# Performance work log

Hardware: AMD Instinct MI355X
Metric: run time of the kernel (lower is better)

The kernel has to match this reference:

```python
import jax, jax.numpy as jnp
import numpy as np

H = 1024      # hidden_dim
P = 8         # n_paths
K = 2         # top_k
THR = 0.1     # firing_threshold
B = 16384     # batch of tokens


def setup_inputs() -> dict:
    key = jax.random.key(0)
    ks = jax.random.split(key, 8)
    g = lambda k, shape, s=0.02: (jax.random.normal(k, shape, dtype=jnp.float32) * s)
    return {
        "x": jax.random.normal(ks[0], (B, H), dtype=jnp.float32),
        # PathGate: Linear(H, H//2) -> SiLU -> Linear(H//2, P), softmax
        "gate_w1": g(ks[1], (H, H // 2)),
        "gate_b1": jnp.zeros((H // 2,), jnp.float32),
        "gate_w2": g(ks[2], (H // 2, P)),
        "gate_b2": jnp.zeros((P,), jnp.float32),
        # each path: Linear(H,H)+SiLU (stacked over P)
        "path_w": g(ks[3], (P, H, H)),
        "path_b": jnp.zeros((P, H), jnp.float32),
        # out_projs: Linear(H,H,bias=False) per path
        "proj_w": g(ks[4], (P, H, H)),
        # blend scalar parameter (init 0.0 -> alpha = 0.5)
        "blend": jnp.zeros((), jnp.float32),
    }


def reference(x, gate_w1, gate_b1, gate_w2, gate_b2, path_w, path_b, proj_w, blend):
    Bn = x.shape[0]
    # gate probabilities (B, P)
    h = jax.nn.silu(x @ gate_w1 + gate_b1)
    gate = jax.nn.softmax(h @ gate_w2 + gate_b2, axis=-1)

    # hard top-k with firing threshold -> per-token per-path combine weight
    vals, idx = jax.lax.top_k(gate, K)              # (B, K)
    fired = vals > THR                              # (B, K)
    w = jnp.zeros_like(gate).at[jnp.arange(Bn)[:, None], idx].add(
        jnp.where(fired, vals, 0.0))                # (B, P) sparse combine weights

    # path compute (dense over P; same values as masked per-path dispatch)
    path_out = jax.nn.silu(jnp.einsum('bh,phd->pbd', x, path_w) + path_b[:, None, :])
    proj_out = jnp.einsum('pbd,pdo->pbo', path_out, proj_w)   # (P, B, H)

    combined = jnp.einsum('bp,pbo->bo', w, proj_out)          # weighted scatter-combine
    total = w.sum(axis=-1)                                    # (B,)
    has_fired = total > 0
    denom = jnp.where(has_fired, total, 1.0)[:, None]
    combined = jnp.where(has_fired[:, None], combined / denom, x)

    alpha = jax.nn.sigmoid(blend)
    out = alpha * combined + (1.0 - alpha) * x
    return out, gate
```

## Files before the change

### kernel.cpp

```cpp
#include <hip/hip_runtime.h>
#include <hip/hip_bf16.h>
#include <cstdint>

#define B_TOK 16384
#define HDIM  1024
#define HGATE 512
#define NPATH 8
#define THRV  0.1f
#define RESSCALE 512.0f
#define MAXROWS (2 * B_TOK + NPATH * 128)

typedef __bf16 bf16x8 __attribute__((ext_vector_type(8)));
typedef _Float16 f16x8 __attribute__((ext_vector_type(8)));
typedef float  f32x4  __attribute__((ext_vector_type(4)));
typedef unsigned short u16;

__device__ __forceinline__ u16 f2bf(float f) {
    uint32_t u = __float_as_uint(f);
    u += 0x7fff + ((u >> 16) & 1);
    return (u16)(u >> 16);
}
__device__ __forceinline__ float bf2f(u16 v) {
    return __uint_as_float((uint32_t)v << 16);
}
union H16 { _Float16 h; u16 u; };
__device__ __forceinline__ u16 f2h(float f) { H16 t; t.h = (_Float16)f; return t.u; }
__device__ __forceinline__ float h2f(u16 b) { H16 t; t.u = b; return (float)t.h; }
__device__ __forceinline__ float silu_f(float a) {
    return a / (1.0f + expf(-a));
}
__device__ __forceinline__ f32x4 mfma_bf16(bf16x8 a, bf16x8 b, f32x4 c) {
    return __builtin_amdgcn_mfma_f32_16x16x32_bf16(a, b, c, 0, 0, 0);
}
__device__ __forceinline__ f32x4 mfma_f16(f16x8 a, f16x8 b, f32x4 c) {
    return __builtin_amdgcn_mfma_f32_16x16x32_f16(a, b, c, 0, 0, 0);
}
__device__ __forceinline__ void async_lds16(const u16* g, u16* l) {
    __builtin_amdgcn_global_load_lds((const __attribute__((address_space(1))) uint32_t*)g,
                                     (__attribute__((address_space(3))) uint32_t*)l,
                                     16, 0, 0);
}

__global__ void k_convert_x(const float* __restrict__ x, u16* __restrict__ xb,
                            u16* __restrict__ xh, u16* __restrict__ xl) {
    int i = (blockIdx.x * 256 + threadIdx.x) * 4;
    float4 v = *(const float4*)(x + i);
    float vv[4] = {v.x, v.y, v.z, v.w};
    u16 hb[4], hh[4], hl[4];
    #pragma unroll
    for (int c = 0; c < 4; c++) {
        hb[c] = f2bf(vv[c]);
        u16 hi = f2h(vv[c]);
        hh[c] = hi;
        hl[c] = f2h((vv[c] - h2f(hi)) * RESSCALE);
    }
    uint2 ob, oh, ol;
    ob.x = (uint32_t)hb[0] | ((uint32_t)hb[1] << 16);
    ob.y = (uint32_t)hb[2] | ((uint32_t)hb[3] << 16);
    oh.x = (uint32_t)hh[0] | ((uint32_t)hh[1] << 16);
    oh.y = (uint32_t)hh[2] | ((uint32_t)hh[3] << 16);
    ol.x = (uint32_t)hl[0] | ((uint32_t)hl[1] << 16);
    ol.y = (uint32_t)hl[2] | ((uint32_t)hl[3] << 16);
    *(uint2*)(xb + i) = ob;
    *(uint2*)(xh + i) = oh;
    *(uint2*)(xl + i) = ol;
}

__global__ void k_transpose_bf16(const float* __restrict__ W, u16* __restrict__ WT) {
    __shared__ float tile[32][33];
    int p = blockIdx.z;
    const float* Wp = W + (size_t)p * HDIM * HDIM;
    u16* WTp = WT + (size_t)p * HDIM * HDIM;
    int d0 = blockIdx.x * 32, h0 = blockIdx.y * 32;
    int tx = threadIdx.x, ty = threadIdx.y;
    #pragma unroll
    for (int rr = 0; rr < 4; rr++) {
        int r = ty + rr * 8;
        tile[r][tx] = Wp[(size_t)(h0 + r) * HDIM + d0 + tx];
    }
    __syncthreads();
    #pragma unroll
    for (int rr = 0; rr < 4; rr++) {
        int r = ty + rr * 8;
        WTp[(size_t)(d0 + r) * HDIM + h0 + tx] = f2bf(tile[tx][r]);
    }
}

__global__ void k_split_w1(const float* __restrict__ W1, u16* __restrict__ WhT,
                           u16* __restrict__ WlT) {
    __shared__ float tile[32][33];
    int n0 = blockIdx.x * 32, k0 = blockIdx.y * 32;
    int tx = threadIdx.x, ty = threadIdx.y;
    #pragma unroll
    for (int rr = 0; rr < 4; rr++) {
        int r = ty + rr * 8;
        tile[r][tx] = W1[(size_t)(k0 + r) * HGATE + n0 + tx];
    }
    __syncthreads();
    #pragma unroll
    for (int rr = 0; rr < 4; rr++) {
        int r = ty + rr * 8;
        float v = tile[tx][r];
        u16 hi = f2h(v);
        WhT[(size_t)(n0 + r) * HDIM + k0 + tx] = hi;
        WlT[(size_t)(n0 + r) * HDIM + k0 + tx] = f2h((v - h2f(hi)) * RESSCALE);
    }
}

__global__ __launch_bounds__(256) void k_gate_mfma(const u16* __restrict__ Ah,
                                                   const u16* __restrict__ Al,
                                                   const u16* __restrict__ BhT,
                                                   const u16* __restrict__ BlT,
                                                   const float* __restrict__ b1,
                                                   float* __restrict__ Hout) {
    __shared__ __align__(16) u16 smem[16384];
    u16* lAh = smem;
    u16* lAl = smem + 4096;
    u16* lBh = smem + 8192;
    u16* lBl = smem + 12288;
    int t = threadIdx.x;
    int n0 = blockIdx.x * 128, m0 = blockIdx.y * 128;
    int wave = t >> 6, lane = t & 63;
    int quad = lane >> 4, l16 = lane & 15;
    int wr = (wave >> 1) * 64, wc = (wave & 1) * 64;
    f32x4 acc[4][4] = {};
    f32x4 accm[4][4] = {};
    union UV { uint4 u; f16x8 v; };
    int c8 = (t & 3) * 8;
    int rb = t >> 2;
    int wb = wave * 512;

    for (int kt = 0; kt < HDIM / 32; kt++) {
        __syncthreads();
        size_t ga0 = (size_t)(m0 + rb) * HDIM + kt * 32 + c8;
        size_t ga1 = (size_t)(m0 + 64 + rb) * HDIM + kt * 32 + c8;
        size_t gb0 = (size_t)(n0 + rb) * HDIM + kt * 32 + c8;
        size_t gb1 = (size_t)(n0 + 64 + rb) * HDIM + kt * 32 + c8;
        async_lds16(Ah + ga0, lAh + wb);
        async_lds16(Ah + ga1, lAh + 2048 + wb);
        async_lds16(Al + ga0, lAl + wb);
        async_lds16(Al + ga1, lAl + 2048 + wb);
        async_lds16(BhT + gb0, lBh + wb);
        async_lds16(BhT + gb1, lBh + 2048 + wb);
        async_lds16(BlT + gb0, lBl + wb);
        async_lds16(BlT + gb1, lBl + 2048 + wb);
        __syncthreads();
        f16x8 avh[4], avl[4], bvh[4], bvl[4];
        #pragma unroll
        for (int i = 0; i < 4; i++) {
            UV u0; u0.u = *(uint4*)(lAh + ((wr + i * 16 + l16) * 32 + quad * 8));
            avh[i] = u0.v;
            UV u1; u1.u = *(uint4*)(lAl + ((wr + i * 16 + l16) * 32 + quad * 8));
            avl[i] = u1.v;
            UV u2; u2.u = *(uint4*)(lBh + ((wc + i * 16 + l16) * 32 + quad * 8));
            bvh[i] = u2.v;
            UV u3; u3.u = *(uint4*)(lBl + ((wc + i * 16 + l16) * 32 + quad * 8));
            bvl[i] = u3.v;
        }
        #pragma unroll
        for (int i = 0; i < 4; i++)
            #pragma unroll
            for (int j = 0; j < 4; j++) {
                acc[i][j]  = mfma_f16(avh[i], bvh[j], acc[i][j]);
                accm[i][j] = mfma_f16(avh[i], bvl[j], accm[i][j]);
                accm[i][j] = mfma_f16(avl[i], bvh[j], accm[i][j]);
            }
    }
    __syncthreads();
    const float inv_s = 1.0f / RESSCALE;
    float* smf = (float*)smem;
    #pragma unroll
    for (int half = 0; half < 2; half++) {
        if ((wave >> 1) == half) {
            #pragma unroll
            for (int j = 0; j < 4; j++) {
                float bj = b1[n0 + wc + j * 16 + l16];
                #pragma unroll
                for (int i = 0; i < 4; i++)
                    #pragma unroll
                    for (int r = 0; r < 4; r++) {
                        int rrow = i * 16 + quad * 4 + r;
                        float v = acc[i][j][r] + accm[i][j][r] * inv_s + bj;
                        smf[rrow * 128 + wc + j * 16 + l16] = silu_f(v);
                    }
            }
        }
        __syncthreads();
        #pragma unroll
        for (int it = 0; it < 8; it++) {
            int c = t + it * 256;
            int row = c >> 5, c4 = (c & 31) * 4;
            *(float4*)(Hout + (size_t)(m0 + half * 64 + row) * HGATE + n0 + c4) =
                *(float4*)(smf + c * 4);
        }
        __syncthreads();
    }
}

__global__ __launch_bounds__(256) void k_gate_topk(const float* __restrict__ Hin,
                                                   const float* __restrict__ W2,
                                                   const float* __restrict__ b2,
                                                   float* __restrict__ gate_out,
                                                   float* __restrict__ wnorm,
                                                   int* __restrict__ counts,
                                                   int* __restrict__ tokens,
                                                   uint32_t* __restrict__ slots) {
    __shared__ float w2t[NPATH * HGATE];
    __shared__ int cnt[NPATH];
    __shared__ int baseS[NPATH];
    __shared__ unsigned short tloc[NPATH][64];
    __shared__ uint32_t sloc[64][2];
    int t = threadIdx.x;
    #pragma unroll
    for (int j = 0; j < 16; j++) {
        int i = t + j * 256;
        w2t[(i & 7) * HGATE + (i >> 3)] = W2[i];
    }
    if (t < NPATH) cnt[t] = 0;
    __syncthreads();
    int wave = t >> 6, lane = t & 63;
    #pragma unroll 1
    for (int it = 0; it < 16; it++) {
        int tl = wave * 16 + it;
        int token = blockIdx.x * 64 + tl;
        const float* hrow = Hin + (size_t)token * HGATE;
        float hv[8];
        {
            float4 h0 = *(const float4*)(hrow + lane * 8);
            float4 h1 = *(const float4*)(hrow + lane * 8 + 4);
            hv[0] = h0.x; hv[1] = h0.y; hv[2] = h0.z; hv[3] = h0.w;
            hv[4] = h1.x; hv[5] = h1.y; hv[6] = h1.z; hv[7] = h1.w;
        }
        float logit[8];
        #pragma unroll
        for (int p = 0; p < 8; p++) {
            float s = 0.0f;
            #pragma unroll
            for (int kk = 0; kk < 8; kk++) s += hv[kk] * w2t[p * HGATE + lane * 8 + kk];
            #pragma unroll
            for (int off = 32; off >= 1; off >>= 1) s += __shfl_xor(s, off);
            logit[p] = s + b2[p];
        }
        float mx = logit[0];
        #pragma unroll
        for (int p = 1; p < 8; p++) mx = fmaxf(mx, logit[p]);
        float pr[8], sum = 0.0f;
        #pragma unroll
        for (int p = 0; p < 8; p++) { pr[p] = expf(logit[p] - mx); sum += pr[p]; }
        float inv = 1.0f / sum;
        #pragma unroll
        for (int p = 0; p < 8; p++) pr[p] *= inv;
        int i0 = 0; float v0 = pr[0];
        #pragma unroll
        for (int p = 1; p < 8; p++) { if (pr[p] > v0) { v0 = pr[p]; i0 = p; } }
        int i1 = -1; float v1 = -1.0f;
        #pragma unroll
        for (int p = 0; p < 8; p++) { if (p != i0 && pr[p] > v1) { v1 = pr[p]; i1 = p; } }
        float w0 = (v0 > THRV) ? v0 : 0.0f;
        float w1 = (v1 > THRV) ? v1 : 0.0f;
        float total = w0 + w1;
        float invden = (total > 0.0f) ? (1.0f / total) : 1.0f;
        if (lane < 8) {
            float prl = pr[0];
            #pragma unroll
            for (int p = 1; p < 8; p++) prl = (lane == p) ? pr[p] : prl;
            float wl = 0.0f;
            if (lane == i0) wl = w0 * invden;
            if (lane == i1) wl = w1 * invden;
            gate_out[(size_t)token * 8 + lane] = prl;
            wnorm[(size_t)token * 8 + lane] = wl;
        }
        if (lane == 0) {
            uint32_t e0 = 0xFFFFFFFFu, e1 = 0xFFFFFFFFu;
            if (w0 > 0.0f) {
                int j0 = atomicAdd(&cnt[i0], 1);
                tloc[i0][j0] = (unsigned short)tl;
                e0 = ((uint32_t)i0 << 16) | (uint32_t)j0;
            }
            if (w1 > 0.0f) {
                int j1 = atomicAdd(&cnt[i1], 1);
                tloc[i1][j1] = (unsigned short)tl;
                e1 = ((uint32_t)i1 << 16) | (uint32_t)j1;
            }
            sloc[tl][0] = e0; sloc[tl][1] = e1;
        }
    }
    __syncthreads();
    if (t < NPATH) baseS[t] = atomicAdd(&counts[t], cnt[t]);
    __syncthreads();
    for (int p = 0; p < NPATH; p++) {
        int n = cnt[p], b = baseS[p];
        for (int j = t; j < n; j += 256)
            tokens[p * B_TOK + b + j] = blockIdx.x * 64 + tloc[p][j];
    }
    if (t < 64) {
        #pragma unroll
        for (int s = 0; s < 2; s++) {
            uint32_t e = sloc[t][s];
            if (e != 0xFFFFFFFFu) {
                int p = e >> 16;
                int j = (int)(e & 0xFFFFu) + baseS[p];
                e = ((uint32_t)p << 16) | (uint32_t)j;
            }
            slots[(size_t)(blockIdx.x * 64 + t) * 2 + s] = e;
        }
    }
}

__global__ void k_prefix(const int* __restrict__ counts, int* __restrict__ poffs) {
    if (threadIdx.x == 0) {
        int o = 0; poffs[0] = 0;
        for (int p = 0; p < NPATH; p++) {
            o += ((counts[p] + 127) >> 7) << 7;
            poffs[p + 1] = o;
        }
    }
}

__global__ __launch_bounds__(256) void k_path1(const u16* __restrict__ A,
                                               const u16* __restrict__ WT,
                                               const float* __restrict__ pb,
                                               u16* __restrict__ hid,
                                               const int* __restrict__ counts,
                                               const int* __restrict__ tokens,
                                               const int* __restrict__ poffs) {
    int p = blockIdx.z;
    int count = counts[p];
    int m0 = blockIdx.y * 128;
    if (m0 >= count) return;
    int n0 = blockIdx.x * 128;
    int base = poffs[p];
    const u16* BT = WT + (size_t)p * HDIM * HDIM;
    const float* bias = pb + (size_t)p * HDIM;

    __shared__ __align__(16) u16 smem[16384];
    __shared__ int idx[128];
    u16* lA = smem;
    u16* lB = smem + 4096;
    int t = threadIdx.x;
    if (t < 128) {
        int j = m0 + t; if (j > count - 1) j = count - 1;
        idx[t] = tokens[p * B_TOK + j];
    }
    __syncthreads();
    int rowA0 = idx[t >> 2], rowA1 = idx[64 + (t >> 2)];
    int wave = t >> 6, lane = t & 63;
    int quad = lane >> 4, l16 = lane & 15;
    int wr = (wave >> 1) * 64, wc = (wave & 1) * 64;
    f32x4 acc[4][4] = {};
    union UV { uint4 u; bf16x8 v; };
    int c8 = (t & 3) * 8;
    int rb = t >> 2;
    int wb = wave * 512;

    for (int kt = 0; kt < HDIM / 32; kt++) {
        __syncthreads();
        async_lds16(A + (size_t)rowA0 * HDIM + kt * 32 + c8, lA + wb);
        async_lds16(A + (size_t)rowA1 * HDIM + kt * 32 + c8, lA + 2048 + wb);
        async_lds16(BT + (size_t)(n0 + rb) * HDIM + kt * 32 + c8, lB + wb);
        async_lds16(BT + (size_t)(n0 + 64 + rb) * HDIM + kt * 32 + c8, lB + 2048 + wb);
        __syncthreads();
        bf16x8 av[4], bv[4];
        #pragma unroll
        for (int i = 0; i < 4; i++) {
            UV ua; ua.u = *(uint4*)(lA + ((wr + i * 16 + l16) * 32 + quad * 8));
            av[i] = ua.v;
            UV ub; ub.u = *(uint4*)(lB + ((wc + i * 16 + l16) * 32 + quad * 8));
            bv[i] = ub.v;
        }
        #pragma unroll
        for (int i = 0; i < 4; i++)
            #pragma unroll
            for (int j = 0; j < 4; j++)
                acc[i][j] = mfma_bf16(av[i], bv[j], acc[i][j]);
    }
    __syncthreads();
    #pragma unroll
    for (int j = 0; j < 4; j++) {
        float bj = bias[n0 + wc + j * 16 + l16];
        #pragma unroll
        for (int i = 0; i < 4; i++)
            #pragma unroll
            for (int r = 0; r < 4; r++) {
                int rrow = wr + i * 16 + quad * 4 + r;
                smem[rrow * 128 + wc + j * 16 + l16] = f2bf(silu_f(acc[i][j][r] + bj));
            }
    }
    __syncthreads();
    #pragma unroll
    for (int it = 0; it < 8; it++) {
        int c = t + it * 256;
        int row = c >> 4, cc = (c & 15) * 8;
        *(uint4*)(hid + (size_t)(base + m0 + row) * HDIM + n0 + cc) = *(uint4*)(smem + c * 8);
    }
}

__global__ __launch_bounds__(256) void k_path2(const u16* __restrict__ hid,
                                               const u16* __restrict__ WT,
                                               const float* __restrict__ wnorm,
                                               u16* __restrict__ pcomp,
                                               const int* __restrict__ counts,
                                               const int* __restrict__ tokens,
                                               const int* __restrict__ poffs) {
    int p = blockIdx.z;
    int count = counts[p];
    int m0 = blockIdx.y * 128;
    if (m0 >= count) return;
    int n0 = blockIdx.x * 128;
    int base = poffs[p];
    const u16* A = hid + (size_t)base * HDIM;
    const u16* BT = WT + (size_t)p * HDIM * HDIM;

    __shared__ __align__(16) u16 smem[16384];
    __shared__ float wv[128];
    u16* lA = smem;
    u16* lB = smem + 4096;
    int t = threadIdx.x;
    if (t < 128) {
        int j = m0 + t; if (j > count - 1) j = count - 1;
        int tok = tokens[p * B_TOK + j];
        wv[t] = wnorm[(size_t)tok * NPATH + p];
    }
    int wave = t >> 6, lane = t & 63;
    int quad = lane >> 4, l16 = lane & 15;
    int wr = (wave >> 1) * 64, wc = (wave & 1) * 64;
    f32x4 acc[4][4] = {};
    union UV { uint4 u; bf16x8 v; };
    int c8 = (t & 3) * 8;
    int rb = t >> 2;
    int wb = wave * 512;

    for (int kt = 0; kt < HDIM / 32; kt++) {
        __syncthreads();
        async_lds16(A + (size_t)(m0 + rb) * HDIM + kt * 32 + c8, lA + wb);
        async_lds16(A + (size_t)(m0 + 64 + rb) * HDIM + kt * 32 + c8, lA + 2048 + wb);
        async_lds16(BT + (size_t)(n0 + rb) * HDIM + kt * 32 + c8, lB + wb);
        async_lds16(BT + (size_t)(n0 + 64 + rb) * HDIM + kt * 32 + c8, lB + 2048 + wb);
        __syncthreads();
        bf16x8 av[4], bv[4];
        #pragma unroll
        for (int i = 0; i < 4; i++) {
            UV ua; ua.u = *(uint4*)(lA + ((wr + i * 16 + l16) * 32 + quad * 8));
            av[i] = ua.v;
            UV ub; ub.u = *(uint4*)(lB + ((wc + i * 16 + l16) * 32 + quad * 8));
            bv[i] = ub.v;
        }
        #pragma unroll
        for (int i = 0; i < 4; i++)
            #pragma unroll
            for (int j = 0; j < 4; j++)
                acc[i][j] = mfma_bf16(av[i], bv[j], acc[i][j]);
    }
    __syncthreads();
    #pragma unroll
    for (int j = 0; j < 4; j++) {
        #pragma unroll
        for (int i = 0; i < 4; i++)
            #pragma unroll
            for (int r = 0; r < 4; r++) {
                int rrow = wr + i * 16 + quad * 4 + r;
                smem[rrow * 128 + wc + j * 16 + l16] = f2bf(wv[rrow] * acc[i][j][r]);
            }
    }
    __syncthreads();
    #pragma unroll
    for (int it = 0; it < 8; it++) {
        int c = t + it * 256;
        int row = c >> 4, cc = (c & 15) * 8;
        *(uint4*)(pcomp + (size_t)(base + m0 + row) * HDIM + n0 + cc) = *(uint4*)(smem + c * 8);
    }
}

__global__ __launch_bounds__(256) void k_blend2(const float* __restrict__ x,
                                                const u16* __restrict__ pcomp,
                                                const uint32_t* __restrict__ slots,
                                                const int* __restrict__ poffs,
                                                const float* __restrict__ blendp,
                                                float* __restrict__ out) {
    int t = threadIdx.x, wave = t >> 6, lane = t & 63;
    int token = blockIdx.x * 4 + wave;
    float alpha = 1.0f / (1.0f + expf(-blendp[0]));
    float beta = 1.0f - alpha;
    uint32_t s0 = slots[(size_t)token * 2];
    uint32_t s1 = slots[(size_t)token * 2 + 1];
    bool f0 = (s0 != 0xFFFFFFFFu), f1 = (s1 != 0xFFFFFFFFu);
    size_t r0 = 0, r1 = 0;
    if (f0) { int p = s0 >> 16, j = s0 & 0xFFFF; r0 = (size_t)(poffs[p] + j) * HDIM; }
    if (f1) { int p = s1 >> 16, j = s1 & 0xFFFF; r1 = (size_t)(poffs[p] + j) * HDIM; }
    const float* xrow = x + (size_t)token * HDIM;
    float* orow = out + (size_t)token * HDIM;
    #pragma unroll
    for (int c = 0; c < 4; c++) {
        int col = c * 256 + lane * 4;
        float4 xv = *(const float4*)(xrow + col);
        float4 o;
        if (f0) {
            uint2 u0 = *(const uint2*)(pcomp + r0 + col);
            float a0 = bf2f(u0.x & 0xFFFF), a1 = bf2f(u0.x >> 16);
            float a2 = bf2f(u0.y & 0xFFFF), a3 = bf2f(u0.y >> 16);
            if (f1) {
                uint2 u1 = *(const uint2*)(pcomp + r1 + col);
                a0 += bf2f(u1.x & 0xFFFF); a1 += bf2f(u1.x >> 16);
                a2 += bf2f(u1.y & 0xFFFF); a3 += bf2f(u1.y >> 16);
            }
            o.x = alpha * a0 + beta * xv.x;
            o.y = alpha * a1 + beta * xv.y;
            o.z = alpha * a2 + beta * xv.z;
            o.w = alpha * a3 + beta * xv.w;
        } else {
            o = xv;
        }
        *(float4*)(orow + col) = o;
    }
}

extern "C" void kernel_launch(void* const* d_in, const int* in_sizes, int n_in,
                              void* d_out, int out_size, void* d_ws, size_t ws_size,
                              hipStream_t stream) {
    const float* x   = (const float*)d_in[0];
    const float* gw1 = (const float*)d_in[1];
    const float* gb1 = (const float*)d_in[2];
    const float* gw2 = (const float*)d_in[3];
    const float* gb2 = (const float*)d_in[4];
    const float* pw  = (const float*)d_in[5];
    const float* pb  = (const float*)d_in[6];
    const float* prw = (const float*)d_in[7];
    const float* blend = (const float*)d_in[8];
    float* out = (float*)d_out;
    float* gate_out = out + (size_t)B_TOK * HDIM;

    char* w = (char*)d_ws;
    size_t o = 0;
    u16* xb      = (u16*)(w + o);   o += (size_t)B_TOK * HDIM * 2;
    u16* pathWT  = (u16*)(w + o);   o += (size_t)NPATH * HDIM * HDIM * 2;
    u16* projWT  = (u16*)(w + o);   o += (size_t)NPATH * HDIM * HDIM * 2;
    u16* w1hT    = (u16*)(w + o);   o += (size_t)HGATE * HDIM * 2;
    u16* w1lT    = (u16*)(w + o);   o += (size_t)HGATE * HDIM * 2;
    size_t uni = o;
    float* hbuf  = (float*)(w + uni);
    u16* pcomp   = (u16*)(w + uni);
    size_t hbuf_sz  = (size_t)B_TOK * HGATE * 4;
    size_t pcomp_sz = (size_t)MAXROWS * HDIM * 2;
    o += (hbuf_sz > pcomp_sz ? hbuf_sz : pcomp_sz);
    size_t uni2 = o;
    u16* xh16    = (u16*)(w + uni2);
    u16* xl16    = (u16*)(w + uni2 + (size_t)B_TOK * HDIM * 2);
    u16* hid     = (u16*)(w + uni2);
    o += (size_t)MAXROWS * HDIM * 2;
    float* wnorm = (float*)(w + o); o += (size_t)B_TOK * NPATH * 4;
    int* tokens  = (int*)(w + o);   o += (size_t)NPATH * B_TOK * 4;
    uint32_t* slots = (uint32_t*)(w + o); o += (size_t)B_TOK * 2 * 4;
    int* counts  = (int*)(w + o);   o += 64;
    int* poffs   = (int*)(w + o);   o += 64;

    hipMemsetAsync(counts, 0, NPATH * sizeof(int), stream);
    k_convert_x<<<dim3((B_TOK * HDIM) / 1024), dim3(256), 0, stream>>>(x, xb, xh16, xl16);
    k_split_w1<<<dim3(HGATE / 32, HDIM / 32), dim3(32, 8), 0, stream>>>(gw1, w1hT, w1lT);
    k_transpose_bf16<<<dim3(32, 32, 8), dim3(32, 8), 0, stream>>>(pw, pathWT);
    k_transpose_bf16<<<dim3(32, 32, 8), dim3(32, 8), 0, stream>>>(prw, projWT);
    k_gate_mfma<<<dim3(HGATE / 128, B_TOK / 128), dim3(256), 0, stream>>>(
        xh16, xl16, w1hT, w1lT, gb1, hbuf);
    k_gate_topk<<<dim3(B_TOK / 64), dim3(256), 0, stream>>>(hbuf, gw2, gb2, gate_out,
                                                            wnorm, counts, tokens, slots);
    k_prefix<<<dim3(1), dim3(64), 0, stream>>>(counts, poffs);
    k_path1<<<dim3(8, 128, 8), dim3(256), 0, stream>>>(xb, pathWT, pb, hid,
                                                       counts, tokens, poffs);
    k_path2<<<dim3(8, 128, 8), dim3(256), 0, stream>>>(hid, projWT, wnorm, pcomp,
                                                       counts, tokens, poffs);
    k_blend2<<<dim3(B_TOK / 4), dim3(256), 0, stream>>>(x, pcomp, slots, poffs, blend, out);
}
```

Measured before the change: 613.0 us.

## Double-buffer LDS tiles in GEMM kernels and swap grid block order

```diff
diff --git a/kernel.cpp b/kernel.cpp
--- a/kernel.cpp
+++ b/kernel.cpp
@@ -113,13 +113,9 @@
                                                    const u16* __restrict__ BlT,
                                                    const float* __restrict__ b1,
                                                    float* __restrict__ Hout) {
-    __shared__ __align__(16) u16 smem[16384];
-    u16* lAh = smem;
-    u16* lAl = smem + 4096;
-    u16* lBh = smem + 8192;
-    u16* lBl = smem + 12288;
+    __shared__ __align__(16) u16 smem[32768];
     int t = threadIdx.x;
-    int n0 = blockIdx.x * 128, m0 = blockIdx.y * 128;
+    int m0 = blockIdx.x * 128, n0 = blockIdx.y * 128;
     int wave = t >> 6, lane = t & 63;
     int quad = lane >> 4, l16 = lane & 15;
     int wr = (wave >> 1) * 64, wc = (wave & 1) * 64;
@@ -130,21 +126,38 @@
     int rb = t >> 2;
     int wb = wave * 512;
 
+    const u16* pAh0 = Ah + (size_t)(m0 + rb) * HDIM + c8;
+    const u16* pAh1 = Ah + (size_t)(m0 + 64 + rb) * HDIM + c8;
+    const u16* pAl0 = Al + (size_t)(m0 + rb) * HDIM + c8;
+    const u16* pAl1 = Al + (size_t)(m0 + 64 + rb) * HDIM + c8;
+    const u16* pBh0 = BhT + (size_t)(n0 + rb) * HDIM + c8;
+    const u16* pBh1 = BhT + (size_t)(n0 + 64 + rb) * HDIM + c8;
+    const u16* pBl0 = BlT + (size_t)(n0 + rb) * HDIM + c8;
+    const u16* pBl1 = BlT + (size_t)(n0 + 64 + rb) * HDIM + c8;
+
+    auto stage = [&](int buf, int kt) {
+        u16* s = smem + buf * 16384;
+        int ko = kt * 32;
+        async_lds16(pAh0 + ko, s + wb);
+        async_lds16(pAh1 + ko, s + 2048 + wb);
+        async_lds16(pAl0 + ko, s + 4096 + wb);
+        async_lds16(pAl1 + ko, s + 6144 + wb);
+        async_lds16(pBh0 + ko, s + 8192 + wb);
+        async_lds16(pBh1 + ko, s + 10240 + wb);
+        async_lds16(pBl0 + ko, s + 12288 + wb);
+        async_lds16(pBl1 + ko, s + 14336 + wb);
+    };
+
+    stage(0, 0);
+    __syncthreads();
+    int cur = 0;
     for (int kt = 0; kt < HDIM / 32; kt++) {
-        __syncthreads();
-        size_t ga0 = (size_t)(m0 + rb) * HDIM + kt * 32 + c8;
-        size_t ga1 = (size_t)(m0 + 64 + rb) * HDIM + kt * 32 + c8;
-        size_t gb0 = (size_t)(n0 + rb) * HDIM + kt * 32 + c8;
-        size_t gb1 = (size_t)(n0 + 64 + rb) * HDIM + kt * 32 + c8;
-        async_lds16(Ah + ga0, lAh + wb);
-        async_lds16(Ah + ga1, lAh + 2048 + wb);
-        async_lds16(Al + ga0, lAl + wb);
-        async_lds16(Al + ga1, lAl + 2048 + wb);
-        async_lds16(BhT + gb0, lBh + wb);
-        async_lds16(BhT + gb1, lBh + 2048 + wb);
-        async_lds16(BlT + gb0, lBl + wb);
-        async_lds16(BlT + gb1, lBl + 2048 + wb);
-        __syncthreads();
+        if (kt + 1 < HDIM / 32) stage(cur ^ 1, kt + 1);
+        u16* s = smem + cur * 16384;
+        u16* lAh = s;
+        u16* lAl = s + 4096;
+        u16* lBh = s + 8192;
+        u16* lBl = s + 12288;
         f16x8 avh[4], avl[4], bvh[4], bvl[4];
         #pragma unroll
         for (int i = 0; i < 4; i++) {
@@ -165,8 +178,9 @@
                 accm[i][j] = mfma_f16(avh[i], bvl[j], accm[i][j]);
                 accm[i][j] = mfma_f16(avl[i], bvh[j], accm[i][j]);
             }
-    }
-    __syncthreads();
+        __syncthreads();
+        cur ^= 1;
+    }
     const float inv_s = 1.0f / RESSCALE;
     float* smf = (float*)smem;
     #pragma unroll
@@ -326,17 +340,15 @@
                                                const int* __restrict__ poffs) {
     int p = blockIdx.z;
     int count = counts[p];
-    int m0 = blockIdx.y * 128;
+    int m0 = blockIdx.x * 128;
     if (m0 >= count) return;
-    int n0 = blockIdx.x * 128;
+    int n0 = blockIdx.y * 128;
     int base = poffs[p];
     const u16* BT = WT + (size_t)p * HDIM * HDIM;
     const float* bias = pb + (size_t)p * HDIM;
 
     __shared__ __align__(16) u16 smem[16384];
     __shared__ int idx[128];
-    u16* lA = smem;
-    u16* lB = smem + 4096;
     int t = threadIdx.x;
     if (t < 128) {
         int j = m0 + t; if (j > count - 1) j = count - 1;
@@ -353,13 +365,27 @@
     int rb = t >> 2;
     int wb = wave * 512;
 
+    const u16* pA0 = A + (size_t)rowA0 * HDIM + c8;
+    const u16* pA1 = A + (size_t)rowA1 * HDIM + c8;
+    const u16* pB0 = BT + (size_t)(n0 + rb) * HDIM + c8;
+    const u16* pB1 = BT + (size_t)(n0 + 64 + rb) * HDIM + c8;
+
+    auto stage = [&](int buf, int kt) {
+        u16* s = smem + buf * 8192;
+        int ko = kt * 32;
+        async_lds16(pA0 + ko, s + wb);
+        async_lds16(pA1 + ko, s + 2048 + wb);
+        async_lds16(pB0 + ko, s + 4096 + wb);
+        async_lds16(pB1 + ko, s + 6144 + wb);
+    };
+
+    stage(0, 0);
+    __syncthreads();
+    int cur = 0;
     for (int kt = 0; kt < HDIM / 32; kt++) {
-        __syncthreads();
-        async_lds16(A + (size_t)rowA0 * HDIM + kt * 32 + c8, lA + wb);
-        async_lds16(A + (size_t)rowA1 * HDIM + kt * 32 + c8, lA + 2048 + wb);
-        async_lds16(BT + (size_t)(n0 + rb) * HDIM + kt * 32 + c8, lB + wb);
-        async_lds16(BT + (size_t)(n0 + 64 + rb) * HDIM + kt * 32 + c8, lB + 2048 + wb);
-        __syncthreads();
+        if (kt + 1 < HDIM / 32) stage(cur ^ 1, kt + 1);
+        u16* lA = smem + cur * 8192;
+        u16* lB = lA + 4096;
         bf16x8 av[4], bv[4];
         #pragma unroll
         for (int i = 0; i < 4; i++) {
@@ -373,8 +399,9 @@
             #pragma unroll
             for (int j = 0; j < 4; j++)
                 acc[i][j] = mfma_bf16(av[i], bv[j], acc[i][j]);
-    }
-    __syncthreads();
+        __syncthreads();
+        cur ^= 1;
+    }
     #pragma unroll
     for (int j = 0; j < 4; j++) {
         float bj = bias[n0 + wc + j * 16 + l16];
@@ -404,17 +431,15 @@
                                                const int* __restrict__ poffs) {
     int p = blockIdx.z;
     int count = counts[p];
-    int m0 = blockIdx.y * 128;
+    int m0 = blockIdx.x * 128;
     if (m0 >= count) return;
-    int n0 = blockIdx.x * 128;
+    int n0 = blockIdx.y * 128;
     int base = poffs[p];
     const u16* A = hid + (size_t)base * HDIM;
     const u16* BT = WT + (size_t)p * HDIM * HDIM;
 
     __shared__ __align__(16) u16 smem[16384];
     __shared__ float wv[128];
-    u16* lA = smem;
-    u16* lB = smem + 4096;
     int t = threadIdx.x;
     if (t < 128) {
         int j = m0 + t; if (j > count - 1) j = count - 1;
@@ -430,13 +455,27 @@
     int rb = t >> 2;
     int wb = wave * 512;
 
+    const u16* pA0 = A + (size_t)(m0 + rb) * HDIM + c8;
+    const u16* pA1 = A + (size_t)(m0 + 64 + rb) * HDIM + c8;
+    const u16* pB0 = BT + (size_t)(n0 + rb) * HDIM + c8;
+    const u16* pB1 = BT + (size_t)(n0 + 64 + rb) * HDIM + c8;
+
+    auto stage = [&](int buf, int kt) {
+        u16* s = smem + buf * 8192;
+        int ko = kt * 32;
+        async_lds16(pA0 + ko, s + wb);
+        async_lds16(pA1 + ko, s + 2048 + wb);
+        async_lds16(pB0 + ko, s + 4096 + wb);
+        async_lds16(pB1 + ko, s + 6144 + wb);
+    };
+
+    stage(0, 0);
+    __syncthreads();
+    int cur = 0;
     for (int kt = 0; kt < HDIM / 32; kt++) {
-        __syncthreads();
-        async_lds16(A + (size_t)(m0 + rb) * HDIM + kt * 32 + c8, lA + wb);
-        async_lds16(A + (size_t)(m0 + 64 + rb) * HDIM + kt * 32 + c8, lA + 2048 + wb);
-        async_lds16(BT + (size_t)(n0 + rb) * HDIM + kt * 32 + c8, lB + wb);
-        async_lds16(BT + (size_t)(n0 + 64 + rb) * HDIM + kt * 32 + c8, lB + 2048 + wb);
-        __syncthreads();
+        if (kt + 1 < HDIM / 32) stage(cur ^ 1, kt + 1);
+        u16* lA = smem + cur * 8192;
+        u16* lB = lA + 4096;
         bf16x8 av[4], bv[4];
         #pragma unroll
         for (int i = 0; i < 4; i++) {
@@ -450,8 +489,9 @@
             #pragma unroll
             for (int j = 0; j < 4; j++)
                 acc[i][j] = mfma_bf16(av[i], bv[j], acc[i][j]);
-    }
-    __syncthreads();
+        __syncthreads();
+        cur ^= 1;
+    }
     #pragma unroll
     for (int j = 0; j < 4; j++) {
         #pragma unroll
@@ -558,14 +598,14 @@
     k_split_w1<<<dim3(HGATE / 32, HDIM / 32), dim3(32, 8), 0, stream>>>(gw1, w1hT, w1lT);
     k_transpose_bf16<<<dim3(32, 32, 8), dim3(32, 8), 0, stream>>>(pw, pathWT);
     k_transpose_bf16<<<dim3(32, 32, 8), dim3(32, 8), 0, stream>>>(prw, projWT);
-    k_gate_mfma<<<dim3(HGATE / 128, B_TOK / 128), dim3(256), 0, stream>>>(
+    k_gate_mfma<<<dim3(B_TOK / 128, HGATE / 128), dim3(256), 0, stream>>>(
         xh16, xl16, w1hT, w1lT, gb1, hbuf);
     k_gate_topk<<<dim3(B_TOK / 64), dim3(256), 0, stream>>>(hbuf, gw2, gb2, gate_out,
                                                             wnorm, counts, tokens, slots);
     k_prefix<<<dim3(1), dim3(64), 0, stream>>>(counts, poffs);
-    k_path1<<<dim3(8, 128, 8), dim3(256), 0, stream>>>(xb, pathWT, pb, hid,
+    k_path1<<<dim3(128, 8, 8), dim3(256), 0, stream>>>(xb, pathWT, pb, hid,
                                                        counts, tokens, poffs);
-    k_path2<<<dim3(8, 128, 8), dim3(256), 0, stream>>>(hid, projWT, wnorm, pcomp,
+    k_path2<<<dim3(128, 8, 8), dim3(256), 0, stream>>>(hid, projWT, wnorm, pcomp,
                                                        counts, tokens, poffs);
     k_blend2<<<dim3(B_TOK / 4), dim3(256), 0, stream>>>(x, pcomp, slots, poffs, blend, out);
 }
```

After: 627.6 us. 2.4% more time.
